# Optimization experiments

Measured on AMD Instinct MI355X. Metric: run time of the kernel, lower is better.

The kernel has to match this reference:

```python
import jax, jax.numpy as jnp
import numpy as np

NUM_HEADS = 8
M = 2
N = 2
OPS = 8      # origin_patch_size
RPS = 16     # resize_patch_size
ED = 768     # embed dim (origin == resize)
HD = ED // NUM_HEADS          # 96 per-head dim
F = ED // NUM_HEADS // 6      # 16 rope freq count
THETA = 10.0
RES = 1024 // RPS             # 64 resize grid
LN_EPS = 1e-5


def _rope_feats(ey, ex):
    # axial 2D RoPE-style positional features: [cos(x*w), sin(x*w), cos(y*w), sin(y*w)] -> (heads, ey*ex, 4F)
    inv = 1.0 / (THETA ** (jnp.arange(F, dtype=jnp.float32) / F))  # (F,)
    ys, xs = jnp.meshgrid(jnp.arange(ey, dtype=jnp.float32),
                          jnp.arange(ex, dtype=jnp.float32), indexing='ij')
    ax = xs.reshape(-1)[:, None] * inv  # (L,F)
    ay = ys.reshape(-1)[:, None] * inv
    feat = jnp.concatenate([jnp.cos(ax), jnp.sin(ax), jnp.cos(ay), jnp.sin(ay)], axis=-1)  # (L,4F)
    return jnp.broadcast_to(feat[None], (NUM_HEADS, ey * ex, 4 * F))


def _window_partition(x, m, n):
    B, H, W, C = x.shape
    wh, ww = H // m, W // n
    x = x.reshape(B, m, wh, n, ww, C).transpose(0, 1, 3, 2, 4, 5).reshape(B * m * n, wh, ww, C)
    return x, wh, ww


def _ln(x, g, b):
    mu = jnp.mean(x, axis=-1, keepdims=True)
    v = jnp.var(x, axis=-1, keepdims=True)
    return (x - mu) / jnp.sqrt(v + LN_EPS) * g + b


def _conv(x, w, b, stride, groups):
    y = jax.lax.conv_general_dilated(x, w, (stride, stride), 'VALID',
                                     dimension_numbers=('NCHW', 'OIHW', 'NCHW'),
                                     feature_group_count=groups)
    return y + b[None, :, None, None]


def _normalize(x):
    n = jnp.sqrt(jnp.sum(x * x, axis=-1, keepdims=True))
    return x / jnp.maximum(n, 1e-12)


def setup_inputs() -> dict:
    key = jax.random.key(0)
    ks = jax.random.split(key, 12)
    s = 0.02
    return {
        'x': jax.random.normal(ks[0], (2, 3, 512, 512), dtype=jnp.float32),
        'origin_w': jax.random.normal(ks[1], (ED, 1, OPS, OPS), dtype=jnp.float32) * s,
        'origin_bias': jnp.zeros((ED,), jnp.float32),
        'resize_w': jax.random.normal(ks[2], (ED, 1, RPS, RPS), dtype=jnp.float32) * s,
        'resize_bias': jnp.zeros((ED,), jnp.float32),
        'pos_embed': jax.random.normal(ks[3], (1, ED, RES, RES), dtype=jnp.float32) * s,
        'nb_g': jnp.ones((ED,), jnp.float32), 'nb_b': jnp.zeros((ED,), jnp.float32),
        'nq_g': jnp.ones((ED,), jnp.float32), 'nq_b': jnp.zeros((ED,), jnp.float32),
        'qw': jax.random.normal(ks[4], (ED, ED), dtype=jnp.float32) * s,
        'qb': jnp.zeros((ED,), jnp.float32),
        'bw': jax.random.normal(ks[5], (ED, ED), dtype=jnp.float32) * s,
        'bb': jnp.zeros((ED,), jnp.float32),
        'projw': jax.random.normal(ks[6], (ED, ED), dtype=jnp.float32) * s,
        'projb': jnp.zeros((ED,), jnp.float32),
    }


def reference(x, origin_w, origin_bias, resize_w, resize_bias, pos_embed,
              nb_g, nb_b, nq_g, nq_b, qw, qb, bw, bb, projw, projb):
    B, C, H, W = x.shape
    rx = jax.image.resize(x, (B, C, 1024, 1024), method='bilinear')
    hp = (OPS - H % OPS) % OPS
    wp = (OPS - W % OPS) % OPS
    x_pad = jnp.pad(x, ((0, 0), (0, 0), (0, hp), (0, wp)))
    op = _conv(x_pad, origin_w, origin_bias, OPS, 3).transpose(0, 2, 3, 1)           # (B,og,og,ED)
    rp = (_conv(rx, resize_w, resize_bias, RPS, 3) + pos_embed).transpose(0, 2, 3, 1)  # (B,64,64,ED)
    op, oh, ow = _window_partition(op, M, N)
    rp, rh, rw = _window_partition(rp, M, N)
    op = _ln(op, nb_g, nb_b)
    rp = _ln(rp, nq_g, nq_b)
    q = rp @ qw.T + qb
    b = op @ bw.T + bb
    Bw = B * M * N
    b = b.reshape(Bw, oh, ow, NUM_HEADS, HD).transpose(0, 3, 1, 2, 4).reshape(Bw, NUM_HEADS, oh * ow, HD)
    q = q.reshape(Bw, rh, rw, NUM_HEADS, HD).transpose(0, 3, 1, 2, 4).reshape(Bw, NUM_HEADS, rh * rw, HD)
    tmp_b = b
    qf = jnp.broadcast_to(_rope_feats(rh, rw)[None], (Bw, NUM_HEADS, rh * rw, 4 * F))
    bf = jnp.broadcast_to(_rope_feats(oh, ow)[None], (Bw, NUM_HEADS, oh * ow, 4 * F))
    q = _normalize(jnp.concatenate([q, qf], axis=-1))
    b = _normalize(jnp.concatenate([b, bf], axis=-1))
    attn = jnp.einsum('bhqd,bhkd->bhqk', q, b)            # cosine-similarity scores (no softmax)
    out = jnp.einsum('bhqk,bhkd->bhqd', attn, tmp_b)      # (Bw, heads, rh*rw, HD)
    out = out.reshape(B, M, N, NUM_HEADS, RES // M, RES // N, HD)
    out = out.transpose(0, 1, 4, 2, 5, 3, 6).reshape(B, RES, RES, ED)
    out = out @ projw.T + projb
    return out.transpose(0, 3, 1, 2), attn
```

## Files before the change

### kernel.cpp

```cpp
#include <hip/hip_runtime.h>
#include <hip/hip_bf16.h>
#include <math.h>


typedef __attribute__((ext_vector_type(8))) short short8;
typedef __attribute__((ext_vector_type(4))) float f32x4;
typedef __attribute__((ext_vector_type(4))) unsigned short us4;

__device__ __forceinline__ unsigned short f2bf(float f) {
    unsigned u = __float_as_uint(f);
    return (unsigned short)((u + 0x7FFFu + ((u >> 16) & 1u)) >> 16);
}
__device__ __forceinline__ float bf2f(unsigned short h) { return __uint_as_float(((unsigned)h) << 16); }
__device__ __forceinline__ void split4(float4 v, us4& h4, us4& l4) {
    unsigned short h0 = f2bf(v.x), h1 = f2bf(v.y), h2 = f2bf(v.z), h3 = f2bf(v.w);
    h4 = (us4){h0, h1, h2, h3};
    l4 = (us4){f2bf(v.x - bf2f(h0)), f2bf(v.y - bf2f(h1)),
               f2bf(v.z - bf2f(h2)), f2bf(v.w - bf2f(h3))};
}

__device__ __forceinline__ void gload16(const unsigned short* g, unsigned short* l)
{
    __builtin_amdgcn_global_load_lds(
        (const __attribute__((address_space(1))) void*)(g),
        (__attribute__((address_space(3))) void*)(l), 16, 0, 0);
}

__global__ __launch_bounds__(256) void k_resize(const float* __restrict__ x, float* __restrict__ rx)
{
    int idx = blockIdx.x * 256 + threadIdx.x;
    int X = idx & 1023;
    int Y = (idx >> 10) & 1023;
    int bc = idx >> 20;
    float sy = Y * 0.5f - 0.25f;
    float sx = X * 0.5f - 0.25f;
    int y0 = (int)floorf(sy), x0 = (int)floorf(sx);
    float fy = sy - (float)y0, fx = sx - (float)x0;
    int y1 = y0 + 1, x1 = x0 + 1;
    y0 = max(0, min(511, y0)); y1 = max(0, min(511, y1));
    x0 = max(0, min(511, x0)); x1 = max(0, min(511, x1));
    const float* p = x + (size_t)bc * (512 * 512);
    float v00 = p[y0 * 512 + x0], v01 = p[y0 * 512 + x1];
    float v10 = p[y1 * 512 + x0], v11 = p[y1 * 512 + x1];
    rx[idx] = (1.f - fy) * ((1.f - fx) * v00 + fx * v01) + fy * ((1.f - fx) * v10 + fx * v11);
}

__global__ void k_rsmall(float* __restrict__ rs)
{
    int e = blockIdx.x * 256 + threadIdx.x;
    if (e >= 63 * 63) return;
    float dy = (float)(e / 63 - 31);
    float dx = (float)(e % 63 - 31);
    float s = 0.f;
    for (int f = 0; f < 16; f++) {
        float invf = powf(10.0f, -(float)f / 16.0f);
        s += cosf(dx * invf) + cosf(dy * invf);
    }
    rs[e] = s;
}

__global__ __launch_bounds__(256) void k_convr(
    const float* __restrict__ rx, const float* __restrict__ wgt,
    const float* __restrict__ bias, const float* __restrict__ pe,
    float* __restrict__ out)
{
    __shared__ float As[16][68];
    __shared__ float Bs[16][68];
    int tid = threadIdx.x;
    int m0 = blockIdx.y * 64;
    int cbase = blockIdx.x * 64;
    int ic = cbase >> 8;
    int ar = tid >> 2, ac = (tid & 3) * 4;
    int ty = tid >> 4, tx = tid & 15;

    int mtok = m0 + ar;
    int w = mtok >> 10, l = mtok & 1023;
    int b = w >> 2, wm = (w >> 1) & 1, wn = w & 1;
    int gy = wm * 32 + (l >> 5), gx = wn * 32 + (l & 31);
    const float* abase = rx + ((size_t)(b * 3 + ic) * 1024 + gy * 16) * 1024 + gx * 16;
    const float* bbase = wgt + (size_t)(cbase + ar) * 256;

    float acc[4][4] = {};
    for (int k0 = 0; k0 < 256; k0 += 16) {
        float4 av = *(const float4*)(abase + (size_t)(k0 >> 4) * 1024 + ac);
        float4 bv = *(const float4*)(bbase + k0 + ac);
        As[ac + 0][ar] = av.x; As[ac + 1][ar] = av.y; As[ac + 2][ar] = av.z; As[ac + 3][ar] = av.w;
        Bs[ac + 0][ar] = bv.x; Bs[ac + 1][ar] = bv.y; Bs[ac + 2][ar] = bv.z; Bs[ac + 3][ar] = bv.w;
        __syncthreads();
#pragma unroll
        for (int k = 0; k < 16; k++) {
            float4 a4 = *(const float4*)&As[k][ty * 4];
            float4 b4 = *(const float4*)&Bs[k][tx * 4];
            float a[4] = {a4.x, a4.y, a4.z, a4.w};
            float bb2[4] = {b4.x, b4.y, b4.z, b4.w};
#pragma unroll
            for (int r = 0; r < 4; r++)
#pragma unroll
                for (int c = 0; c < 4; c++) acc[r][c] += a[r] * bb2[c];
        }
        __syncthreads();
    }
#pragma unroll
    for (int r = 0; r < 4; r++) {
        int t = m0 + ty * 4 + r;
        int tw = t >> 10, tl = t & 1023;
        int tgy = ((tw >> 1) & 1) * 32 + (tl >> 5);
        int tgx = (tw & 1) * 32 + (tl & 31);
#pragma unroll
        for (int c = 0; c < 4; c++) {
            int cc = cbase + tx * 4 + c;
            out[(size_t)t * 768 + cc] = acc[r][c] + bias[cc] + pe[(size_t)cc * 4096 + tgy * 64 + tgx];
        }
    }
}

__global__ __launch_bounds__(256) void k_convo(
    const float* __restrict__ x, const float* __restrict__ wgt,
    const float* __restrict__ bias, float* __restrict__ out)
{
    __shared__ float As[16][68];
    __shared__ float Bs[16][68];
    int tid = threadIdx.x;
    int m0 = blockIdx.y * 64;
    int cbase = blockIdx.x * 64;
    int ic = cbase >> 8;
    int ar = tid >> 2, ac = (tid & 3) * 4;
    int ty = tid >> 4, tx = tid & 15;

    int mtok = m0 + ar;
    int w = mtok >> 10, l = mtok & 1023;
    int b = w >> 2, wm = (w >> 1) & 1, wn = w & 1;
    int gy = wm * 32 + (l >> 5), gx = wn * 32 + (l & 31);
    const float* abase = x + ((size_t)(b * 3 + ic) * 512 + gy * 8) * 512 + gx * 8;
    const float* bbase = wgt + (size_t)(cbase + ar) * 64;

    float acc[4][4] = {};
    for (int k0 = 0; k0 < 64; k0 += 16) {
        int k = k0 + ac;
        float4 av = *(const float4*)(abase + (size_t)(k >> 3) * 512 + (k & 7));
        float4 bv = *(const float4*)(bbase + k);
        As[ac + 0][ar] = av.x; As[ac + 1][ar] = av.y; As[ac + 2][ar] = av.z; As[ac + 3][ar] = av.w;
        Bs[ac + 0][ar] = bv.x; Bs[ac + 1][ar] = bv.y; Bs[ac + 2][ar] = bv.z; Bs[ac + 3][ar] = bv.w;
        __syncthreads();
#pragma unroll
        for (int k2 = 0; k2 < 16; k2++) {
            float4 a4 = *(const float4*)&As[k2][ty * 4];
            float4 b4 = *(const float4*)&Bs[k2][tx * 4];
            float a[4] = {a4.x, a4.y, a4.z, a4.w};
            float bb2[4] = {b4.x, b4.y, b4.z, b4.w};
#pragma unroll
            for (int r = 0; r < 4; r++)
#pragma unroll
                for (int c = 0; c < 4; c++) acc[r][c] += a[r] * bb2[c];
        }
        __syncthreads();
    }
#pragma unroll
    for (int r = 0; r < 4; r++) {
        int t = m0 + ty * 4 + r;
#pragma unroll
        for (int c = 0; c < 4; c++) {
            int cc = cbase + tx * 4 + c;
            out[(size_t)t * 768 + cc] = acc[r][c] + bias[cc];
        }
    }
}

__global__ __launch_bounds__(256) void k_ln_pack(
    const float* __restrict__ in, const float* __restrict__ g,
    const float* __restrict__ beta, unsigned short* __restrict__ oh,
    unsigned short* __restrict__ ol)
{
    int blk = blockIdx.x;
    int tid = threadIdx.x;
    __shared__ float redA[256], redB[256];
    float v[3];
#pragma unroll
    for (int r = 0; r < 3; r++) v[r] = in[(size_t)blk * 768 + r * 256 + tid];
    float s = v[0] + v[1] + v[2];
    float sq = v[0] * v[0] + v[1] * v[1] + v[2] * v[2];
    redA[tid] = s; redB[tid] = sq;
    __syncthreads();
    for (int off = 128; off > 0; off >>= 1) {
        if (tid < off) { redA[tid] += redA[tid + off]; redB[tid] += redB[tid + off]; }
        __syncthreads();
    }
    float mu = redA[0] * (1.0f / 768.0f);
    float var = redB[0] * (1.0f / 768.0f) - mu * mu;
    float rstd = rsqrtf(var + 1e-5f);
#pragma unroll
    for (int r = 0; r < 3; r++) {
        int c = r * 256 + tid;
        float y = (v[r] - mu) * rstd * g[c] + beta[c];
        unsigned short hv = f2bf(y);
        oh[(size_t)blk * 768 + c] = hv;
        ol[(size_t)blk * 768 + c] = f2bf(y - bf2f(hv));
    }
}

__global__ __launch_bounds__(256) void k_packw(
    const float* __restrict__ src, unsigned short* __restrict__ dh,
    unsigned short* __restrict__ dl, int n4)
{
    int idx = blockIdx.x * 256 + threadIdx.x;
    if (idx >= n4) return;
    float4 v = ((const float4*)src)[idx];
    us4 h, l; split4(v, h, l);
    ((us4*)dh)[idx] = h;
    ((us4*)dl)[idx] = l;
}

__global__ __launch_bounds__(256) void k_norm(
    const float* __restrict__ qbuf, const float* __restrict__ bbuf,
    float* __restrict__ qinv, float* __restrict__ binv)
{
    int blk = blockIdx.x;
    int tid = threadIdx.x;
    int which = blk >> 13;
    int row = blk & 8191;
    const float* src = (which ? bbuf : qbuf) + (size_t)row * 768;
    float* dst = which ? binv : qinv;
    __shared__ float sq[768];
#pragma unroll
    for (int r = 0; r < 3; r++) { int c = r * 256 + tid; float vv = src[c]; sq[c] = vv * vv; }
    __syncthreads();
    if (tid < 8) {
        float s = 32.0f;
        const float* p = sq + tid * 96;
#pragma unroll
        for (int d = 0; d < 96; d++) s += p[d];
        int w = row >> 10, l = row & 1023;
        dst[(size_t)(w * 8 + tid) * 1024 + l] = rsqrtf(s);
    }
}

__global__ __launch_bounds__(256) void k_packq(
    const float* __restrict__ src, unsigned short* __restrict__ dh, unsigned short* __restrict__ dl)
{
    int idx = blockIdx.x * 256 + threadIdx.x;
    int dq = idx % 24;
    int rest = idx / 24;
    int l = rest & 1023, z = rest >> 10;
    int w = z >> 3, h = z & 7;
    float4 v = *(const float4*)(src + (size_t)((w << 10) + l) * 768 + h * 96 + dq * 4);
    us4 hv, lv; split4(v, hv, lv);
    size_t o = ((size_t)(z << 10) + l) * 96 + dq * 4;
    *(us4*)(dh + o) = hv;
    *(us4*)(dl + o) = lv;
}

__global__ __launch_bounds__(256) void k_packb(
    const float* __restrict__ src, unsigned short* __restrict__ dh, unsigned short* __restrict__ dl,
    unsigned short* __restrict__ th, unsigned short* __restrict__ tl)
{
    __shared__ float T[128][97];
    int z = blockIdx.x >> 3, lt = blockIdx.x & 7;
    int w = z >> 3, h = z & 7;
    int tid = threadIdx.x;
#pragma unroll
    for (int rq = 0; rq < 12; rq++) {
        int q = rq * 256 + tid;
        int l = q / 24, dq = (q % 24) * 4;
        float4 v = *(const float4*)(src + (size_t)((w << 10) + lt * 128 + l) * 768 + h * 96 + dq);
        us4 hv, lv; split4(v, hv, lv);
        size_t o = ((size_t)(z << 10) + lt * 128 + l) * 96 + dq;
        *(us4*)(dh + o) = hv;
        *(us4*)(dl + o) = lv;
        T[l][dq + 0] = v.x; T[l][dq + 1] = v.y; T[l][dq + 2] = v.z; T[l][dq + 3] = v.w;
    }
    __syncthreads();
#pragma unroll
    for (int rq = 0; rq < 12; rq++) {
        int q = rq * 256 + tid;
        int d = q >> 5, lq = (q & 31) * 4;
        float4 v = make_float4(T[lq + 0][d], T[lq + 1][d], T[lq + 2][d], T[lq + 3][d]);
        us4 hv, lv; split4(v, hv, lv);
        size_t o = ((size_t)z * 96 + d) * 1024 + lt * 128 + lq;
        *(us4*)(th + o) = hv;
        *(us4*)(tl + o) = lv;
    }
}

__device__ __forceinline__ void mfma_block44(
    short8 afh[4], short8 afl[4], short8 bfh[4], short8 bfl[4], f32x4 acc[4][4])
{
#pragma unroll
    for (int mi = 0; mi < 4; mi++)
#pragma unroll
        for (int ni = 0; ni < 4; ni++) {
            f32x4 c = acc[mi][ni];
            c = __builtin_amdgcn_mfma_f32_16x16x32_bf16(afh[mi], bfh[ni], c, 0, 0, 0);
            c = __builtin_amdgcn_mfma_f32_16x16x32_bf16(afh[mi], bfl[ni], c, 0, 0, 0);
            c = __builtin_amdgcn_mfma_f32_16x16x32_bf16(afl[mi], bfh[ni], c, 0, 0, 0);
            acc[mi][ni] = c;
        }
}


__device__ __forceinline__ void stage_tile(
    const unsigned short* __restrict__ src, unsigned short* lbuf,
    int mbase, int K, int kofs, int tid)
{
    int row = tid >> 2;
    int kc  = tid & 3;
    int v   = (row >> 1) & 3;
    int kcs = (kc ^ v) << 3;
#pragma unroll
    for (int j = 0; j < 2; j++) {
        int r = row + j * 64;
        const unsigned short* g = src + (size_t)(mbase + r) * K + kofs + kcs;
        gload16(g, lbuf + r * 32 + (kc << 3));
    }
}

__device__ __forceinline__ void stage4(
    const unsigned short* __restrict__ Ah, const unsigned short* __restrict__ Al,
    const unsigned short* __restrict__ Bh, const unsigned short* __restrict__ Bl,
    unsigned short* lds_stage, int m0, int n0, int K, int kofs, int tid)
{
    stage_tile(Ah, lds_stage,         m0, K, kofs, tid);
    stage_tile(Al, lds_stage + 4096,  m0, K, kofs, tid);
    stage_tile(Bh, lds_stage + 8192,  n0, K, kofs, tid);
    stage_tile(Bl, lds_stage + 12288, n0, K, kofs, tid);
}

__device__ __forceinline__ void frags_from_lds(
    const unsigned short* lds_stage, int wm, int wn, int lrow, int lgrp,
    short8 afh[4], short8 afl[4], short8 bfh[4], short8 bfl[4])
{
    int ch = (lgrp ^ ((lrow >> 1) & 3)) * 8;
    const unsigned short* Ah = lds_stage;
    const unsigned short* Al = lds_stage + 4096;
    const unsigned short* Bh = lds_stage + 8192;
    const unsigned short* Bl = lds_stage + 12288;
#pragma unroll
    for (int mi = 0; mi < 4; mi++) {
        int row = wm * 64 + mi * 16 + lrow;
        afh[mi] = *(const short8*)(Ah + row * 32 + ch);
        afl[mi] = *(const short8*)(Al + row * 32 + ch);
    }
#pragma unroll
    for (int ni = 0; ni < 4; ni++) {
        int row = wn * 64 + ni * 16 + lrow;
        bfh[ni] = *(const short8*)(Bh + row * 32 + ch);
        bfl[ni] = *(const short8*)(Bl + row * 32 + ch);
    }
}

__device__ __forceinline__ void gemm_lds_core(
    const unsigned short* __restrict__ Ah, const unsigned short* __restrict__ Al,
    const unsigned short* __restrict__ Bh, const unsigned short* __restrict__ Bl,
    unsigned short* lds, int m0, int n0, int K, f32x4 acc[4][4])
{
    int tid = threadIdx.x, lane = tid & 63, wid = tid >> 6;
    int wm = wid >> 1, wn = wid & 1, lrow = lane & 15, lgrp = lane >> 4;
    int nkt = K >> 5;
    stage4(Ah, Al, Bh, Bl, lds, m0, n0, K, 0, tid);
    __syncthreads();
    for (int kt = 0; kt < nkt; kt++) {
        int cur = kt & 1;
        if (kt + 1 < nkt)
            stage4(Ah, Al, Bh, Bl, lds + (cur ^ 1) * 16384, m0, n0, K, (kt + 1) << 5, tid);
        short8 afh[4], afl[4], bfh[4], bfl[4];
        frags_from_lds(lds + cur * 16384, wm, wn, lrow, lgrp, afh, afl, bfh, bfl);
        mfma_block44(afh, afl, bfh, bfl, acc);
        __syncthreads();
    }
}

__global__ __launch_bounds__(256) void k_gemm_mfma_bias(
    const unsigned short* __restrict__ Ah, const unsigned short* __restrict__ Al,
    const unsigned short* __restrict__ Bh, const unsigned short* __restrict__ Bl,
    const float* __restrict__ bias, float* __restrict__ C)
{
    __shared__ unsigned short lds[2][16384];
    int tid = threadIdx.x, lane = tid & 63, wid = tid >> 6;
    int wm = wid >> 1, wn = wid & 1;
    int lrow = lane & 15, lgrp = lane >> 4;
    int m0 = blockIdx.y * 128, n0 = blockIdx.x * 128;
    f32x4 acc[4][4] = {};
    gemm_lds_core(Ah, Al, Bh, Bl, &lds[0][0], m0, n0, 768, acc);

    int ibase = m0 + wm * 64 + lgrp * 4;
    int jbase = n0 + wn * 64 + lrow;
#pragma unroll
    for (int ni = 0; ni < 4; ni++) {
        int j = jbase + ni * 16;
        float bj = bias[j];
#pragma unroll
        for (int mi = 0; mi < 4; mi++) {
            int ib = ibase + mi * 16;
#pragma unroll
            for (int r = 0; r < 4; r++)
                C[(size_t)(ib + r) * 768 + j] = acc[mi][ni][r] + bj;
        }
    }
}

__global__ __launch_bounds__(256) void k_proj_mfma(
    const unsigned short* __restrict__ Ah, const unsigned short* __restrict__ Al,
    const unsigned short* __restrict__ Bh, const unsigned short* __restrict__ Bl,
    const float* __restrict__ pb, float* __restrict__ out0)
{
    __shared__ unsigned short lds[2][16384];
    int tid = threadIdx.x, lane = tid & 63, wid = tid >> 6;
    int wm = wid >> 1, wn = wid & 1;
    int lrow = lane & 15, lgrp = lane >> 4;
    int m0 = blockIdx.y * 128, n0 = blockIdx.x * 128;
    f32x4 acc[4][4] = {};
    gemm_lds_core(Ah, Al, Bh, Bl, &lds[0][0], m0, n0, 768, acc);

    int ibase = m0 + wm * 64 + lgrp * 4;
    int jbase = n0 + wn * 64 + lrow;
#pragma unroll
    for (int ni = 0; ni < 4; ni++) {
        int cc = jbase + ni * 16;
        float bj = pb[cc];
        float* obase = out0 + (size_t)cc * 4096;
#pragma unroll
        for (int mi = 0; mi < 4; mi++) {
            int i0 = ibase + mi * 16;
            float4 v = make_float4(acc[mi][ni][0] + bj, acc[mi][ni][1] + bj,
                                   acc[mi][ni][2] + bj, acc[mi][ni][3] + bj);
            *(float4*)(obase + (size_t)(i0 >> 12) * 3145728 + (i0 & 4095)) = v;
        }
    }
}

__global__ __launch_bounds__(256) void k_attn_mfma(
    const unsigned short* __restrict__ qh_, const unsigned short* __restrict__ ql_,
    const unsigned short* __restrict__ bh_, const unsigned short* __restrict__ bl_,
    const float* __restrict__ qinv, const float* __restrict__ binv,
    const float* __restrict__ rs, float* __restrict__ attn)
{
    __shared__ unsigned short lds[2][16384];
    int z = blockIdx.z;
    int n0 = blockIdx.x * 128, m0 = blockIdx.y * 128;
    int tid = threadIdx.x;
    int lane = tid & 63, wid = tid >> 6;
    int wm = wid >> 1, wn = wid & 1;
    int lrow = lane & 15, lgrp = lane >> 4;

    size_t zoff = (size_t)z * 1024 * 96;
    f32x4 acc[4][4] = {};
    gemm_lds_core(qh_ + zoff, ql_ + zoff, bh_ + zoff, bl_ + zoff,
                  &lds[0][0], m0, n0, 96, acc);

    float* Cz = attn + ((size_t)z << 20);
    const float* qiz = qinv + (z << 10);
    const float* biz = binv + (z << 10);
    int ibase = m0 + wm * 64 + lgrp * 4;
    int jbase = n0 + wn * 64 + lrow;

    float qv[16];
#pragma unroll
    for (int mi = 0; mi < 4; mi++)
#pragma unroll
        for (int r = 0; r < 4; r++) qv[mi * 4 + r] = qiz[ibase + mi * 16 + r];

#pragma unroll
    for (int ni = 0; ni < 4; ni++) {
        int j = jbase + ni * 16;
        float bj = biz[j];
        int jy = j >> 5, jx = j & 31;
#pragma unroll
        for (int mi = 0; mi < 4; mi++) {
#pragma unroll
            for (int r = 0; r < 4; r++) {
                int i = ibase + mi * 16 + r;
                int dy = (i >> 5) - jy + 31;
                int dx = (i & 31) - jx + 31;
                Cz[(size_t)i * 1024 + j] = (acc[mi][ni][r] + rs[dy * 63 + dx]) * qv[mi * 4 + r] * bj;
            }
        }
    }
}

__device__ __forceinline__ void stage_cvt_write(
    unsigned short (*Ah)[40], unsigned short (*Al)[40], int srow, int skb,
    float4 a, float4 b, float4 c, float4 d)
{
    us4 h0, l0, h1, l1, h2, l2, h3, l3;
    split4(a, h0, l0); split4(b, h1, l1); split4(c, h2, l2); split4(d, h3, l3);
    *(us4*)&Ah[srow][skb + 0]  = h0; *(us4*)&Al[srow][skb + 0]  = l0;
    *(us4*)&Ah[srow][skb + 4]  = h1; *(us4*)&Al[srow][skb + 4]  = l1;
    *(us4*)&Ah[srow][skb + 8]  = h2; *(us4*)&Al[srow][skb + 8]  = l2;
    *(us4*)&Ah[srow][skb + 12] = h3; *(us4*)&Al[srow][skb + 12] = l3;
}

__global__ __launch_bounds__(256) void k_out_mfma(
    const float* __restrict__ attn, const unsigned short* __restrict__ bth,
    const unsigned short* __restrict__ btl, unsigned short* __restrict__ tokh,
    unsigned short* __restrict__ tokl)
{
    __shared__ unsigned short AhS[2][128][40];
    __shared__ unsigned short AlS[2][128][40];
    int z = blockIdx.z, m0 = blockIdx.y * 128;
    int w = z >> 3, h = z & 7;
    int tid = threadIdx.x, lane = tid & 63, wid = tid >> 6;
    int lrow = lane & 15, lgrp = lane >> 4;

    const float* A = attn + ((size_t)z << 20) + (size_t)m0 * 1024;
    const unsigned short* Bh = bth + (size_t)z * 98304;
    const unsigned short* Bl = btl + (size_t)z * 98304;

    int srow = tid >> 1, skb = (tid & 1) * 16;
    const float* sp = A + (size_t)srow * 1024 + skb;

    f32x4 acc[2][6] = {};

    float4 sv0 = *(const float4*)(sp + 0);
    float4 sv1 = *(const float4*)(sp + 4);
    float4 sv2 = *(const float4*)(sp + 8);
    float4 sv3 = *(const float4*)(sp + 12);
    stage_cvt_write(AhS[0], AlS[0], srow, skb, sv0, sv1, sv2, sv3);
    __syncthreads();

    for (int kt = 0; kt < 32; kt++) {
        int cur = kt & 1;
        if (kt < 31) {
            const float* p = sp + (kt + 1) * 32;
            sv0 = *(const float4*)(p + 0);
            sv1 = *(const float4*)(p + 4);
            sv2 = *(const float4*)(p + 8);
            sv3 = *(const float4*)(p + 12);
        }
        short8 bfh[6], bfl[6];
#pragma unroll
        for (int ni = 0; ni < 6; ni++) {
            size_t o = (size_t)(ni * 16 + lrow) * 1024 + kt * 32 + lgrp * 8;
            bfh[ni] = *(const short8*)(Bh + o);
            bfl[ni] = *(const short8*)(Bl + o);
        }
        short8 afh[2], afl[2];
#pragma unroll
        for (int mi = 0; mi < 2; mi++) {
            int r = wid * 32 + mi * 16 + lrow;
            afh[mi] = *(const short8*)&AhS[cur][r][lgrp * 8];
            afl[mi] = *(const short8*)&AlS[cur][r][lgrp * 8];
        }
#pragma unroll
        for (int mi = 0; mi < 2; mi++)
#pragma unroll
            for (int ni = 0; ni < 6; ni++) {
                f32x4 c = acc[mi][ni];
                c = __builtin_amdgcn_mfma_f32_16x16x32_bf16(afh[mi], bfh[ni], c, 0, 0, 0);
                c = __builtin_amdgcn_mfma_f32_16x16x32_bf16(afh[mi], bfl[ni], c, 0, 0, 0);
                c = __builtin_amdgcn_mfma_f32_16x16x32_bf16(afl[mi], bfh[ni], c, 0, 0, 0);
                acc[mi][ni] = c;
            }
        if (kt < 31) stage_cvt_write(AhS[cur ^ 1], AlS[cur ^ 1], srow, skb, sv0, sv1, sv2, sv3);
        __syncthreads();
    }

    int b = w >> 2, wm = (w >> 1) & 1, wn = w & 1;
#pragma unroll
    for (int mi = 0; mi < 2; mi++) {
#pragma unroll
        for (int r = 0; r < 4; r++) {
            int i = m0 + wid * 32 + mi * 16 + lgrp * 4 + r;
            int t = (b * 64 + wm * 32 + (i >> 5)) * 64 + wn * 32 + (i & 31);
            size_t base = (size_t)t * 768 + h * 96;
#pragma unroll
            for (int ni = 0; ni < 6; ni++) {
                float v = acc[mi][ni][r];
                unsigned short hv = f2bf(v);
                tokh[base + ni * 16 + lrow] = hv;
                tokl[base + ni * 16 + lrow] = f2bf(v - bf2f(hv));
            }
        }
    }
}

extern "C" void kernel_launch(void* const* d_in, const int* in_sizes, int n_in,
                              void* d_out, int out_size, void* d_ws, size_t ws_size,
                              hipStream_t stream)
{
    const float* x   = (const float*)d_in[0];
    const float* ow  = (const float*)d_in[1];
    const float* ob  = (const float*)d_in[2];
    const float* rw  = (const float*)d_in[3];
    const float* rb  = (const float*)d_in[4];
    const float* pe  = (const float*)d_in[5];
    const float* nbg = (const float*)d_in[6];
    const float* nbb = (const float*)d_in[7];
    const float* nqg = (const float*)d_in[8];
    const float* nqb = (const float*)d_in[9];
    const float* qw  = (const float*)d_in[10];
    const float* qb  = (const float*)d_in[11];
    const float* bw  = (const float*)d_in[12];
    const float* bb  = (const float*)d_in[13];
    const float* pw  = (const float*)d_in[14];
    const float* pb  = (const float*)d_in[15];

    float* out0 = (float*)d_out;
    float* attn = out0 + 6291456;

    float* ws   = (float*)d_ws;
    float* rx   = ws;
    float* slot1 = ws + 1 * 6291456;
    float* slot2 = ws + 2 * 6291456;
    float* slot3 = ws + 3 * 6291456;
    float* slot4 = ws + 4 * 6291456;
    float* qinv = ws + 5 * 6291456;
    float* binv = qinv + 65536;
    float* rs   = binv + 65536;

    float* rpre = slot3;
    float* opre = slot4;
    float* qbuf = slot3;
    float* bbuf = slot4;

    unsigned short* rlnh = (unsigned short*)slot2;
    unsigned short* rlnl = rlnh + 6291456;
    unsigned short* olnh = (unsigned short*)slot1;
    unsigned short* olnl = olnh + 6291456;

    unsigned short* qwh = (unsigned short*)rx;
    unsigned short* qwl = qwh + 589824;
    unsigned short* bwh = qwh + 2 * 589824;
    unsigned short* bwl = qwh + 3 * 589824;
    unsigned short* pwh = (unsigned short*)slot4;
    unsigned short* pwl = pwh + 589824;

    unsigned short* qh  = (unsigned short*)slot2;
    unsigned short* ql  = qh + 6291456;
    unsigned short* bh2 = (unsigned short*)slot1;
    unsigned short* bl2 = bh2 + 6291456;
    unsigned short* bth = (unsigned short*)slot3;
    unsigned short* btl = bth + 6291456;

    unsigned short* tokh = (unsigned short*)rx;
    unsigned short* tokl = tokh + 6291456;

    k_resize<<<24576, 256, 0, stream>>>(x, rx);
    k_rsmall<<<16, 256, 0, stream>>>(rs);

    dim3 gc(12, 128);
    k_convr<<<gc, 256, 0, stream>>>(rx, rw, rb, pe, rpre);
    k_packw<<<576, 256, 0, stream>>>(qw, qwh, qwl, 147456);
    k_packw<<<576, 256, 0, stream>>>(bw, bwh, bwl, 147456);
    k_convo<<<gc, 256, 0, stream>>>(x, ow, ob, opre);

    k_ln_pack<<<8192, 256, 0, stream>>>(rpre, nqg, nqb, rlnh, rlnl);
    k_ln_pack<<<8192, 256, 0, stream>>>(opre, nbg, nbb, olnh, olnl);

    dim3 gg(6, 64);
    k_gemm_mfma_bias<<<gg, 256, 0, stream>>>(rlnh, rlnl, qwh, qwl, qb, qbuf);
    k_gemm_mfma_bias<<<gg, 256, 0, stream>>>(olnh, olnl, bwh, bwl, bb, bbuf);

    k_norm<<<16384, 256, 0, stream>>>(qbuf, bbuf, qinv, binv);

    k_packq<<<6144, 256, 0, stream>>>(qbuf, qh, ql);
    k_packb<<<512, 256, 0, stream>>>(bbuf, bh2, bl2, bth, btl);
    k_packw<<<576, 256, 0, stream>>>(pw, pwh, pwl, 147456);

    dim3 ga(8, 8, 64);
    k_attn_mfma<<<ga, 256, 0, stream>>>(qh, ql, bh2, bl2, qinv, binv, rs, attn);

    dim3 go(1, 8, 64);
    k_out_mfma<<<go, 256, 0, stream>>>(attn, bth, btl, tokh, tokl);

    k_proj_mfma<<<gg, 256, 0, stream>>>(tokh, tokl, pwh, pwl, pb, out0);
}
```

Before: 796.1 us.

## Move patch-embed convs to split-bf16 MFMA, stage attn stores, retile out GEMM

Replaces the two FP32 SIMT grouped-conv GEMMs with an im2col pack into hi/lo bf16 halves plus the shared MFMA GEMM core, with a fused bias and pos-embed epilogue. The attention-score epilogue now writes to an LDS tile and stores rows coalesced to global memory. The out GEMM halves its M tile to 64 rows per block, doubling the grid. The pack kernels add extra memory passes and workspace traffic in exchange for running the conv GEMMs on matrix cores.

After: 824.5 us. +3.6%, slower.

```diff
diff --git a/kernel.cpp b/kernel.cpp
--- a/kernel.cpp
+++ b/kernel.cpp
@@ -59,111 +59,40 @@
     rs[e] = s;
 }
 
-__global__ __launch_bounds__(256) void k_convr(
-    const float* __restrict__ rx, const float* __restrict__ wgt,
-    const float* __restrict__ bias, const float* __restrict__ pe,
-    float* __restrict__ out)
-{
-    __shared__ float As[16][68];
-    __shared__ float Bs[16][68];
-    int tid = threadIdx.x;
-    int m0 = blockIdx.y * 64;
-    int cbase = blockIdx.x * 64;
-    int ic = cbase >> 8;
-    int ar = tid >> 2, ac = (tid & 3) * 4;
-    int ty = tid >> 4, tx = tid & 15;
-
-    int mtok = m0 + ar;
-    int w = mtok >> 10, l = mtok & 1023;
+__global__ __launch_bounds__(256) void k_packim_r(
+    const float* __restrict__ rx, unsigned short* __restrict__ dh, unsigned short* __restrict__ dl)
+{
+    int idx = blockIdx.x * 256 + threadIdx.x;
+    int c = idx >> 19;
+    int rest = idx & 524287;
+    int t = rest >> 6, qk = rest & 63;
+    int k = qk * 4, py = k >> 4, px = k & 15;
+    int w = t >> 10, l = t & 1023;
     int b = w >> 2, wm = (w >> 1) & 1, wn = w & 1;
     int gy = wm * 32 + (l >> 5), gx = wn * 32 + (l & 31);
-    const float* abase = rx + ((size_t)(b * 3 + ic) * 1024 + gy * 16) * 1024 + gx * 16;
-    const float* bbase = wgt + (size_t)(cbase + ar) * 256;
-
-    float acc[4][4] = {};
-    for (int k0 = 0; k0 < 256; k0 += 16) {
-        float4 av = *(const float4*)(abase + (size_t)(k0 >> 4) * 1024 + ac);
-        float4 bv = *(const float4*)(bbase + k0 + ac);
-        As[ac + 0][ar] = av.x; As[ac + 1][ar] = av.y; As[ac + 2][ar] = av.z; As[ac + 3][ar] = av.w;
-        Bs[ac + 0][ar] = bv.x; Bs[ac + 1][ar] = bv.y; Bs[ac + 2][ar] = bv.z; Bs[ac + 3][ar] = bv.w;
-        __syncthreads();
-#pragma unroll
-        for (int k = 0; k < 16; k++) {
-            float4 a4 = *(const float4*)&As[k][ty * 4];
-            float4 b4 = *(const float4*)&Bs[k][tx * 4];
-            float a[4] = {a4.x, a4.y, a4.z, a4.w};
-            float bb2[4] = {b4.x, b4.y, b4.z, b4.w};
-#pragma unroll
-            for (int r = 0; r < 4; r++)
-#pragma unroll
-                for (int c = 0; c < 4; c++) acc[r][c] += a[r] * bb2[c];
-        }
-        __syncthreads();
-    }
-#pragma unroll
-    for (int r = 0; r < 4; r++) {
-        int t = m0 + ty * 4 + r;
-        int tw = t >> 10, tl = t & 1023;
-        int tgy = ((tw >> 1) & 1) * 32 + (tl >> 5);
-        int tgx = (tw & 1) * 32 + (tl & 31);
-#pragma unroll
-        for (int c = 0; c < 4; c++) {
-            int cc = cbase + tx * 4 + c;
-            out[(size_t)t * 768 + cc] = acc[r][c] + bias[cc] + pe[(size_t)cc * 4096 + tgy * 64 + tgx];
-        }
-    }
-}
-
-__global__ __launch_bounds__(256) void k_convo(
-    const float* __restrict__ x, const float* __restrict__ wgt,
-    const float* __restrict__ bias, float* __restrict__ out)
-{
-    __shared__ float As[16][68];
-    __shared__ float Bs[16][68];
-    int tid = threadIdx.x;
-    int m0 = blockIdx.y * 64;
-    int cbase = blockIdx.x * 64;
-    int ic = cbase >> 8;
-    int ar = tid >> 2, ac = (tid & 3) * 4;
-    int ty = tid >> 4, tx = tid & 15;
-
-    int mtok = m0 + ar;
-    int w = mtok >> 10, l = mtok & 1023;
+    float4 v = *(const float4*)(rx + ((size_t)(b * 3 + c) << 20) + (size_t)(gy * 16 + py) * 1024 + gx * 16 + px);
+    us4 hv, lv; split4(v, hv, lv);
+    size_t o = ((size_t)(c << 13) + t) * 256 + k;
+    *(us4*)(dh + o) = hv;
+    *(us4*)(dl + o) = lv;
+}
+
+__global__ __launch_bounds__(256) void k_packim_o(
+    const float* __restrict__ x, unsigned short* __restrict__ dh, unsigned short* __restrict__ dl)
+{
+    int idx = blockIdx.x * 256 + threadIdx.x;
+    int c = idx >> 17;
+    int rest = idx & 131071;
+    int t = rest >> 4, qk = rest & 15;
+    int k = qk * 4, py = k >> 3, px = k & 7;
+    int w = t >> 10, l = t & 1023;
     int b = w >> 2, wm = (w >> 1) & 1, wn = w & 1;
     int gy = wm * 32 + (l >> 5), gx = wn * 32 + (l & 31);
-    const float* abase = x + ((size_t)(b * 3 + ic) * 512 + gy * 8) * 512 + gx * 8;
-    const float* bbase = wgt + (size_t)(cbase + ar) * 64;
-
-    float acc[4][4] = {};
-    for (int k0 = 0; k0 < 64; k0 += 16) {
-        int k = k0 + ac;
-        float4 av = *(const float4*)(abase + (size_t)(k >> 3) * 512 + (k & 7));
-        float4 bv = *(const float4*)(bbase + k);
-        As[ac + 0][ar] = av.x; As[ac + 1][ar] = av.y; As[ac + 2][ar] = av.z; As[ac + 3][ar] = av.w;
-        Bs[ac + 0][ar] = bv.x; Bs[ac + 1][ar] = bv.y; Bs[ac + 2][ar] = bv.z; Bs[ac + 3][ar] = bv.w;
-        __syncthreads();
-#pragma unroll
-        for (int k2 = 0; k2 < 16; k2++) {
-            float4 a4 = *(const float4*)&As[k2][ty * 4];
-            float4 b4 = *(const float4*)&Bs[k2][tx * 4];
-            float a[4] = {a4.x, a4.y, a4.z, a4.w};
-            float bb2[4] = {b4.x, b4.y, b4.z, b4.w};
-#pragma unroll
-            for (int r = 0; r < 4; r++)
-#pragma unroll
-                for (int c = 0; c < 4; c++) acc[r][c] += a[r] * bb2[c];
-        }
-        __syncthreads();
-    }
-#pragma unroll
-    for (int r = 0; r < 4; r++) {
-        int t = m0 + ty * 4 + r;
-#pragma unroll
-        for (int c = 0; c < 4; c++) {
-            int cc = cbase + tx * 4 + c;
-            out[(size_t)t * 768 + cc] = acc[r][c] + bias[cc];
-        }
-    }
+    float4 v = *(const float4*)(x + ((size_t)(b * 3 + c) << 18) + (size_t)(gy * 8 + py) * 512 + gx * 8 + px);
+    us4 hv, lv; split4(v, hv, lv);
+    size_t o = ((size_t)(c << 13) + t) * 64 + k;
+    *(us4*)(dh + o) = hv;
+    *(us4*)(dl + o) = lv;
 }
 
 __global__ __launch_bounds__(256) void k_ln_pack(
@@ -397,6 +326,68 @@
     }
 }
 
+__device__ __forceinline__ void conv_epilogue(
+    f32x4 acc[4][4], const float* __restrict__ bias, const float* __restrict__ pe,
+    float* __restrict__ out, int m0, int n0, int wm, int wn, int lrow, int lgrp)
+{
+    int ibase = m0 + wm * 64 + lgrp * 4;
+    int jbase = n0 + wn * 64 + lrow;
+#pragma unroll
+    for (int ni = 0; ni < 4; ni++) {
+        int cc = jbase + ni * 16;
+        float bj = bias[cc];
+#pragma unroll
+        for (int mi = 0; mi < 4; mi++) {
+#pragma unroll
+            for (int r = 0; r < 4; r++) {
+                int t = ibase + mi * 16 + r;
+                float val = acc[mi][ni][r] + bj;
+                if (pe) {
+                    int tw = t >> 10, tl = t & 1023;
+                    int tgy = ((tw >> 1) & 1) * 32 + (tl >> 5);
+                    int tgx = (tw & 1) * 32 + (tl & 31);
+                    val += pe[(size_t)cc * 4096 + tgy * 64 + tgx];
+                }
+                out[(size_t)t * 768 + cc] = val;
+            }
+        }
+    }
+}
+
+__global__ __launch_bounds__(256) void k_convr_mfma(
+    const unsigned short* __restrict__ Ah, const unsigned short* __restrict__ Al,
+    const unsigned short* __restrict__ Bh, const unsigned short* __restrict__ Bl,
+    const float* __restrict__ bias, const float* __restrict__ pe, float* __restrict__ out)
+{
+    __shared__ unsigned short lds[2][16384];
+    int tid = threadIdx.x, lane = tid & 63, wid = tid >> 6;
+    int wm = wid >> 1, wn = wid & 1;
+    int lrow = lane & 15, lgrp = lane >> 4;
+    int m0 = blockIdx.y * 128, n0 = blockIdx.x * 128;
+    int g = n0 >> 8;
+    size_t go = (size_t)g * 8192 * 256;
+    f32x4 acc[4][4] = {};
+    gemm_lds_core(Ah + go, Al + go, Bh, Bl, &lds[0][0], m0, n0, 256, acc);
+    conv_epilogue(acc, bias, pe, out, m0, n0, wm, wn, lrow, lgrp);
+}
+
+__global__ __launch_bounds__(256) void k_convo_mfma(
+    const unsigned short* __restrict__ Ah, const unsigned short* __restrict__ Al,
+    const unsigned short* __restrict__ Bh, const unsigned short* __restrict__ Bl,
+    const float* __restrict__ bias, float* __restrict__ out)
+{
+    __shared__ unsigned short lds[2][16384];
+    int tid = threadIdx.x, lane = tid & 63, wid = tid >> 6;
+    int wm = wid >> 1, wn = wid & 1;
+    int lrow = lane & 15, lgrp = lane >> 4;
+    int m0 = blockIdx.y * 128, n0 = blockIdx.x * 128;
+    int g = n0 >> 8;
+    size_t go = (size_t)g * 8192 * 64;
+    f32x4 acc[4][4] = {};
+    gemm_lds_core(Ah + go, Al + go, Bh, Bl, &lds[0][0], m0, n0, 64, acc);
+    conv_epilogue(acc, bias, (const float*)nullptr, out, m0, n0, wm, wn, lrow, lgrp);
+}
+
 __global__ __launch_bounds__(256) void k_proj_mfma(
     const unsigned short* __restrict__ Ah, const unsigned short* __restrict__ Al,
     const unsigned short* __restrict__ Bh, const unsigned short* __restrict__ Bl,
@@ -433,7 +424,8 @@
     const float* __restrict__ qinv, const float* __restrict__ binv,
     const float* __restrict__ rs, float* __restrict__ attn)
 {
-    __shared__ unsigned short lds[2][16384];
+    __shared__ __align__(16) float Sx[128][130];
+    unsigned short* lds = (unsigned short*)&Sx[0][0];
     int z = blockIdx.z;
     int n0 = blockIdx.x * 128, m0 = blockIdx.y * 128;
     int tid = threadIdx.x;
@@ -444,9 +436,8 @@
     size_t zoff = (size_t)z * 1024 * 96;
     f32x4 acc[4][4] = {};
     gemm_lds_core(qh_ + zoff, ql_ + zoff, bh_ + zoff, bl_ + zoff,
-                  &lds[0][0], m0, n0, 96, acc);
-
-    float* Cz = attn + ((size_t)z << 20);
+                  lds, m0, n0, 96, acc);
+
     const float* qiz = qinv + (z << 10);
     const float* biz = binv + (z << 10);
     int ibase = m0 + wm * 64 + lgrp * 4;
@@ -463,6 +454,7 @@
         int j = jbase + ni * 16;
         float bj = biz[j];
         int jy = j >> 5, jx = j & 31;
+        int jl = wn * 64 + ni * 16 + lrow;
 #pragma unroll
         for (int mi = 0; mi < 4; mi++) {
 #pragma unroll
@@ -470,22 +462,20 @@
                 int i = ibase + mi * 16 + r;
                 int dy = (i >> 5) - jy + 31;
                 int dx = (i & 31) - jx + 31;
-                Cz[(size_t)i * 1024 + j] = (acc[mi][ni][r] + rs[dy * 63 + dx]) * qv[mi * 4 + r] * bj;
+                int il = wm * 64 + lgrp * 4 + mi * 16 + r;
+                Sx[il][jl] = (acc[mi][ni][r] + rs[dy * 63 + dx]) * qv[mi * 4 + r] * bj;
             }
         }
     }
-}
-
-__device__ __forceinline__ void stage_cvt_write(
-    unsigned short (*Ah)[40], unsigned short (*Al)[40], int srow, int skb,
-    float4 a, float4 b, float4 c, float4 d)
-{
-    us4 h0, l0, h1, l1, h2, l2, h3, l3;
-    split4(a, h0, l0); split4(b, h1, l1); split4(c, h2, l2); split4(d, h3, l3);
-    *(us4*)&Ah[srow][skb + 0]  = h0; *(us4*)&Al[srow][skb + 0]  = l0;
-    *(us4*)&Ah[srow][skb + 4]  = h1; *(us4*)&Al[srow][skb + 4]  = l1;
-    *(us4*)&Ah[srow][skb + 8]  = h2; *(us4*)&Al[srow][skb + 8]  = l2;
-    *(us4*)&Ah[srow][skb + 12] = h3; *(us4*)&Al[srow][skb + 12] = l3;
+    __syncthreads();
+
+    float* Cz = attn + ((size_t)z << 20);
+#pragma unroll
+    for (int rr = 0; rr < 32; rr++) {
+        int row = wid * 32 + rr;
+        float2 v = *(const float2*)&Sx[row][lane * 2];
+        *(float2*)(Cz + (size_t)(m0 + row) * 1024 + n0 + lane * 2) = v;
+    }
 }
 
 __global__ __launch_bounds__(256) void k_out_mfma(
@@ -493,9 +483,9 @@
     const unsigned short* __restrict__ btl, unsigned short* __restrict__ tokh,
     unsigned short* __restrict__ tokl)
 {
-    __shared__ unsigned short AhS[2][128][40];
-    __shared__ unsigned short AlS[2][128][40];
-    int z = blockIdx.z, m0 = blockIdx.y * 128;
+    __shared__ unsigned short AhS[2][64][40];
+    __shared__ unsigned short AlS[2][64][40];
+    int z = blockIdx.z, m0 = blockIdx.y * 64;
     int w = z >> 3, h = z & 7;
     int tid = threadIdx.x, lane = tid & 63, wid = tid >> 6;
     int lrow = lane & 15, lgrp = lane >> 4;
@@ -504,16 +494,19 @@
     const unsigned short* Bh = bth + (size_t)z * 98304;
     const unsigned short* Bl = btl + (size_t)z * 98304;
 
-    int srow = tid >> 1, skb = (tid & 1) * 16;
+    int srow = tid >> 2, skb = (tid & 3) * 8;
     const float* sp = A + (size_t)srow * 1024 + skb;
 
-    f32x4 acc[2][6] = {};
+    f32x4 acc6[6] = {};
 
     float4 sv0 = *(const float4*)(sp + 0);
     float4 sv1 = *(const float4*)(sp + 4);
-    float4 sv2 = *(const float4*)(sp + 8);
-    float4 sv3 = *(const float4*)(sp + 12);
-    stage_cvt_write(AhS[0], AlS[0], srow, skb, sv0, sv1, sv2, sv3);
+    {
+        us4 h0, l0, h1, l1;
+        split4(sv0, h0, l0); split4(sv1, h1, l1);
+        *(us4*)&AhS[0][srow][skb + 0] = h0; *(us4*)&AhS[0][srow][skb + 4] = h1;
+        *(us4*)&AlS[0][srow][skb + 0] = l0; *(us4*)&AlS[0][srow][skb + 4] = l1;
+    }
     __syncthreads();
 
     for (int kt = 0; kt < 32; kt++) {
@@ -522,8 +515,6 @@
             const float* p = sp + (kt + 1) * 32;
             sv0 = *(const float4*)(p + 0);
             sv1 = *(const float4*)(p + 4);
-            sv2 = *(const float4*)(p + 8);
-            sv3 = *(const float4*)(p + 12);
         }
         short8 bfh[6], bfl[6];
 #pragma unroll
@@ -532,42 +523,37 @@
             bfh[ni] = *(const short8*)(Bh + o);
             bfl[ni] = *(const short8*)(Bl + o);
         }
-        short8 afh[2], afl[2];
-#pragma unroll
-        for (int mi = 0; mi < 2; mi++) {
-            int r = wid * 32 + mi * 16 + lrow;
-            afh[mi] = *(const short8*)&AhS[cur][r][lgrp * 8];
-            afl[mi] = *(const short8*)&AlS[cur][r][lgrp * 8];
-        }
-#pragma unroll
-        for (int mi = 0; mi < 2; mi++)
-#pragma unroll
-            for (int ni = 0; ni < 6; ni++) {
-                f32x4 c = acc[mi][ni];
-                c = __builtin_amdgcn_mfma_f32_16x16x32_bf16(afh[mi], bfh[ni], c, 0, 0, 0);
-                c = __builtin_amdgcn_mfma_f32_16x16x32_bf16(afh[mi], bfl[ni], c, 0, 0, 0);
-                c = __builtin_amdgcn_mfma_f32_16x16x32_bf16(afl[mi], bfh[ni], c, 0, 0, 0);
-                acc[mi][ni] = c;
-            }
-        if (kt < 31) stage_cvt_write(AhS[cur ^ 1], AlS[cur ^ 1], srow, skb, sv0, sv1, sv2, sv3);
+        short8 afh = *(const short8*)&AhS[cur][wid * 16 + lrow][lgrp * 8];
+        short8 afl = *(const short8*)&AlS[cur][wid * 16 + lrow][lgrp * 8];
+#pragma unroll
+        for (int ni = 0; ni < 6; ni++) {
+            f32x4 c = acc6[ni];
+            c = __builtin_amdgcn_mfma_f32_16x16x32_bf16(afh, bfh[ni], c, 0, 0, 0);
+            c = __builtin_amdgcn_mfma_f32_16x16x32_bf16(afh, bfl[ni], c, 0, 0, 0);
+            c = __builtin_amdgcn_mfma_f32_16x16x32_bf16(afl, bfh[ni], c, 0, 0, 0);
+            acc6[ni] = c;
+        }
+        if (kt < 31) {
+            us4 h0, l0, h1, l1;
+            split4(sv0, h0, l0); split4(sv1, h1, l1);
+            *(us4*)&AhS[cur ^ 1][srow][skb + 0] = h0; *(us4*)&AhS[cur ^ 1][srow][skb + 4] = h1;
+            *(us4*)&AlS[cur ^ 1][srow][skb + 0] = l0; *(us4*)&AlS[cur ^ 1][srow][skb + 4] = l1;
+        }
         __syncthreads();
     }
 
     int b = w >> 2, wm = (w >> 1) & 1, wn = w & 1;
 #pragma unroll
-    for (int mi = 0; mi < 2; mi++) {
-#pragma unroll
-        for (int r = 0; r < 4; r++) {
-            int i = m0 + wid * 32 + mi * 16 + lgrp * 4 + r;
-            int t = (b * 64 + wm * 32 + (i >> 5)) * 64 + wn * 32 + (i & 31);
-            size_t base = (size_t)t * 768 + h * 96;
-#pragma unroll
-            for (int ni = 0; ni < 6; ni++) {
-                float v = acc[mi][ni][r];
-                unsigned short hv = f2bf(v);
-                tokh[base + ni * 16 + lrow] = hv;
-                tokl[base + ni * 16 + lrow] = f2bf(v - bf2f(hv));
-            }
+    for (int r = 0; r < 4; r++) {
+        int i = m0 + wid * 16 + lgrp * 4 + r;
+        int t = (b * 64 + wm * 32 + (i >> 5)) * 64 + wn * 32 + (i & 31);
+        size_t base = (size_t)t * 768 + h * 96;
+#pragma unroll
+        for (int ni = 0; ni < 6; ni++) {
+            float v = acc6[ni][r];
+            unsigned short hv = f2bf(v);
+            tokh[base + ni * 16 + lrow] = hv;
+            tokl[base + ni * 16 + lrow] = f2bf(v - bf2f(hv));
         }
     }
 }
@@ -611,6 +597,11 @@
     float* qbuf = slot3;
     float* bbuf = slot4;
 
+    unsigned short* rimh = (unsigned short*)slot2;
+    unsigned short* riml = rimh + 6291456;
+    unsigned short* oimh = (unsigned short*)slot1;
+    unsigned short* oiml = oimh + 1572864;
+
     unsigned short* rlnh = (unsigned short*)slot2;
     unsigned short* rlnl = rlnh + 6291456;
     unsigned short* olnh = (unsigned short*)slot1;
@@ -620,6 +611,10 @@
     unsigned short* qwl = qwh + 589824;
     unsigned short* bwh = qwh + 2 * 589824;
     unsigned short* bwl = qwh + 3 * 589824;
+    unsigned short* rwph = qwh + 4 * 589824;
+    unsigned short* rwpl = rwph + 196608;
+    unsigned short* owph = rwph + 2 * 196608;
+    unsigned short* owpl = owph + 49152;
     unsigned short* pwh = (unsigned short*)slot4;
     unsigned short* pwl = pwh + 589824;
 
@@ -636,16 +631,20 @@
     k_resize<<<24576, 256, 0, stream>>>(x, rx);
     k_rsmall<<<16, 256, 0, stream>>>(rs);
 
-    dim3 gc(12, 128);
-    k_convr<<<gc, 256, 0, stream>>>(rx, rw, rb, pe, rpre);
+    k_packim_r<<<6144, 256, 0, stream>>>(rx, rimh, riml);
+    k_packim_o<<<1536, 256, 0, stream>>>(x, oimh, oiml);
     k_packw<<<576, 256, 0, stream>>>(qw, qwh, qwl, 147456);
     k_packw<<<576, 256, 0, stream>>>(bw, bwh, bwl, 147456);
-    k_convo<<<gc, 256, 0, stream>>>(x, ow, ob, opre);
+    k_packw<<<192, 256, 0, stream>>>(rw, rwph, rwpl, 49152);
+    k_packw<<<48, 256, 0, stream>>>(ow, owph, owpl, 12288);
+
+    dim3 gg(6, 64);
+    k_convr_mfma<<<gg, 256, 0, stream>>>(rimh, riml, rwph, rwpl, rb, pe, rpre);
+    k_convo_mfma<<<gg, 256, 0, stream>>>(oimh, oiml, owph, owpl, ob, opre);
 
     k_ln_pack<<<8192, 256, 0, stream>>>(rpre, nqg, nqb, rlnh, rlnl);
     k_ln_pack<<<8192, 256, 0, stream>>>(opre, nbg, nbb, olnh, olnl);
 
-    dim3 gg(6, 64);
     k_gemm_mfma_bias<<<gg, 256, 0, stream>>>(rlnh, rlnl, qwh, qwl, qb, qbuf);
     k_gemm_mfma_bias<<<gg, 256, 0, stream>>>(olnh, olnl, bwh, bwl, bb, bbuf);
 
@@ -658,7 +657,7 @@
     dim3 ga(8, 8, 64);
     k_attn_mfma<<<ga, 256, 0, stream>>>(qh, ql, bh2, bl2, qinv, binv, rs, attn);
 
-    dim3 go(1, 8, 64);
+    dim3 go(1, 16, 64);
     k_out_mfma<<<go, 256, 0, stream>>>(attn, bth, btl, tokh, tokl);
 
     k_proj_mfma<<<gg, 256, 0, stream>>>(tokh, tokl, pwh, pwl, pb, out0);
```
